# Optimization experiments

Measured on AMD Instinct MI355X. Metric: run time of the kernel, lower is better.

The kernel has to match this reference:

```python
import jax, jax.numpy as jnp
import numpy as np

C = 256       # channels (MWI ctor arg c)
K = 8         # number of EM bases (MWI ctor arg k)
STAGES = 7    # EM iterations per scale (stage_num)
SIZES = (1, 3, 5)  # multi-scale unfold kernel sizes


def _unfold(x, k):
    # torch F.unfold(x, k, padding=(k-1)//2, stride=1) -> (b, c, k*k, h, w)
    # with kernel-position ordering (ki major, kj minor), matching torch layout.
    b, c, h, w = x.shape
    p = (k - 1) // 2
    xp = jnp.pad(x, ((0, 0), (0, 0), (p, p), (p, p)))
    pats = [xp[:, :, i:i + h, j:j + w] for i in range(k) for j in range(k)]
    return jnp.stack(pats, axis=2)


def _fold(z, k, h, w):
    # inverse of _unfold with overlap-add: z (b, c, k*k, h, w) -> (b, c, h, w)
    b, c, kk, _, _ = z.shape
    p = (k - 1) // 2
    out = jnp.zeros((b, c, h + 2 * p, w + 2 * p), z.dtype)
    for idx in range(kk):
        i, j = divmod(idx, k)
        out = out.at[:, :, i:i + h, j:j + w].add(z[:, :, idx])
    return out[:, :, p:p + h, p:p + w]


def _l2norm(v, axis):
    return v / (1e-6 + jnp.linalg.norm(v, axis=axis, keepdims=True))


def setup_inputs() -> dict:
    key = jax.random.key(0)
    k0, k1, k2 = jax.random.split(key, 3)
    b, h, w = 4, 64, 64
    x = jax.random.normal(k0, (b, C, h, w), jnp.float32)
    # mu buffer: normal(0, sqrt(2/k)) then l2-normalized over channel dim
    mu0 = jax.random.normal(k1, (1, C, K), jnp.float32) * np.float32(np.sqrt(2.0 / K))
    mu0 = _l2norm(mu0, axis=1)
    w_scale = jnp.float32(1.0)
    # convcat: Conv2d(3c, c, 1) init normal(0, sqrt(2/(1*1*out_channels)))
    convcat_w = jax.random.normal(k2, (C, 3 * C, 1, 1), jnp.float32) * np.float32(np.sqrt(2.0 / C))
    convcat_b = jnp.zeros((C,), jnp.float32)
    return {"x": x, "mu0": mu0, "w_scale": w_scale,
            "convcat_w": convcat_w, "convcat_b": convcat_b}


def reference(x, mu0, w_scale, convcat_w, convcat_b):
    b, c, h, w = x.shape
    idn = x
    # EM iterations run under torch.no_grad(): stop gradients through mu/z.
    mu = jax.lax.stop_gradient(jnp.broadcast_to(mu0, (b, c, K)))
    feats = []
    for size in SIZES:
        uf = _unfold(x, size).reshape(b, c, -1)          # (b, c, n), n = size^2*h*w
        uf_sg = jax.lax.stop_gradient(uf)
        z = None
        for _ in range(STAGES):
            z = jax.nn.softmax(jnp.einsum('bcn,bck->bnk', uf_sg, mu), axis=2)
            z_ = z / (1e-6 + z.sum(axis=1, keepdims=True))
            mu = _l2norm(jnp.einsum('bcn,bnk->bck', uf_sg, z_), axis=1)
        # reconstruction: mu @ z^T -> (b, c, n), fold back with overlap-add
        zr = jnp.einsum('bck,bnk->bcn', mu, z).reshape(b, c, size * size, h, w)
        feats.append(_fold(zr, size, h, w))
    cat = jnp.concatenate(feats, axis=1)                 # (b, 3c, h, w)
    u = jnp.einsum('bihw,oi->bohw', cat, convcat_w[:, :, 0, 0]) \
        + convcat_b[None, :, None, None]
    out = jax.nn.relu(u * w_scale + idn)
    return out, mu
```

## Files before the change

### kernel.cpp

```cpp
#include <hip/hip_runtime.h>
#include <hip/hip_bf16.h>

#define KB 8


__device__ __forceinline__ float bf16_to_f(unsigned short u) {
    union { unsigned int i; float f; } v;
    v.i = ((unsigned int)u) << 16;
    return v.f;
}

__device__ __forceinline__ unsigned short f_to_bf16_bits(float f) {
    __hip_bfloat16 h = (__hip_bfloat16)f;
    return *(unsigned short*)&h;
}

__device__ __forceinline__ float wf(int i, int pd) {
    return (float)(min(pd, i) + min(pd, 63 - i) + 1);
}

__global__ __launch_bounds__(256)
void probe_all_kernel(const unsigned short* __restrict__ x,
                      const unsigned short* __restrict__ mu0,
                      const unsigned short* __restrict__ Wc,
                      int* __restrict__ slots)
{
    __shared__ unsigned int red[256];
    int bid = blockIdx.x, t = threadIdx.x;
    const unsigned short* p;
    int n;
    if (bid < 32)       { p = x + bid * 2048;         n = 2048; }
    else if (bid == 32) { p = mu0;                    n = 2048; }
    else                { p = Wc + (bid - 33) * 4096; n = 4096; }
    unsigned int mx = 0;
    for (int i = t; i < n; i += 256) {
        unsigned int bits = (((unsigned int)p[i]) << 16) & 0x7FFFFFFFu;
        mx = max(mx, bits);
    }
    red[t] = mx;
    __syncthreads();
    for (int st = 128; st > 0; st >>= 1) {
        if (t < st) red[t] = max(red[t], red[t + st]);
        __syncthreads();
    }
    if (t == 0) slots[bid] = (int)red[0];
}

__global__ __launch_bounds__(256)
void decide_init_kernel(const unsigned short* __restrict__ wsc_u,
                        const void* __restrict__ mu0,
                        int* __restrict__ slots,
                        float* __restrict__ muInit)
{
    int t = threadIdx.x;
    if (t == 0) {
        const int TH = 0x49742400;
        int mxX = 0, mxW = 0;
        for (int i = 0; i < 32; ++i)  mxX = max(mxX, slots[i]);
        for (int i = 33; i < 49; ++i) mxW = max(mxW, slots[i]);
        slots[56] = (mxX < TH) ? 1 : 0;
        slots[57] = (slots[32] < TH) ? 1 : 0;
        slots[58] = (mxW < TH) ? 1 : 0;
        slots[59] = (bf16_to_f(wsc_u[0]) == 1.0f) ? 1 : 0;
    }
    __syncthreads();
    int fb = slots[57];
    const unsigned short* mb = (const unsigned short*)mu0;
    const float*          mf = (const float*)mu0;
    for (int i = t; i < 2048; i += 256)
        muInit[i] = fb ? bf16_to_f(mb[i]) : mf[i];
}

__global__ __launch_bounds__(512)
void stage_z_kernel(const void* __restrict__ x,
                    unsigned short* __restrict__ xbf,
                    const float* __restrict__ inst,
                    const float* __restrict__ muInit,
                    const void* __restrict__ Wc,
                    float* __restrict__ Mg,
                    float* __restrict__ pp,
                    float* __restrict__ pps,
                    __hip_bfloat16* __restrict__ zfOut,
                    const int* __restrict__ flags,
                    int pd, float oobPrev, int mode, int writeM, int sM,
                    int writeXbf)
{
    __shared__ __hip_bfloat16 xt[256][66];
    __shared__ float muL[2048];
    __shared__ float pr[4608];
    __shared__ float zws[512];
    __shared__ float muRed[32];
    __shared__ float sS[8][8];

    const int tid = threadIdx.x;
    const int bid = blockIdx.x;
    const int b   = bid >> 6;
    const int row = bid & 63;
    const int p0  = row << 6;
    const int fW  = flags[2];

    if (!writeXbf) {
        #pragma unroll
        for (int i = 0; i < 4; ++i) {
            int idx = tid + i * 512;
            int c = idx >> 3, sub = idx & 7;
            const uint4 u = *(const uint4*)(xbf
                          + ((size_t)(b * 256 + c) << 12) + (size_t)(p0 + sub * 8));
            unsigned int* d = (unsigned int*)((unsigned short*)&xt[c][0] + sub * 8);
            d[0] = u.x; d[1] = u.y; d[2] = u.z; d[3] = u.w;
        }
    } else if (flags[0]) {
        #pragma unroll
        for (int i = 0; i < 4; ++i) {
            int idx = tid + i * 512;
            int c = idx >> 3, sub = idx & 7;
            size_t gb = ((size_t)(b * 256 + c) << 12) + (size_t)(p0 + sub * 8);
            const uint4 u = *(const uint4*)((const unsigned short*)x + gb);
            unsigned int* d = (unsigned int*)((unsigned short*)&xt[c][0] + sub * 8);
            d[0] = u.x; d[1] = u.y; d[2] = u.z; d[3] = u.w;
            *(uint4*)(xbf + gb) = u;
        }
    } else {
        #pragma unroll
        for (int i = 0; i < 8; ++i) {
            int idx = tid + i * 512;
            int c = idx >> 4, sub = idx & 15;
            size_t gb = ((size_t)(b * 256 + c) << 12) + (size_t)(p0 + sub * 4);
            const float4 a = *(const float4*)((const float*)x + gb);
            unsigned int u0 = ((unsigned int)f_to_bf16_bits(a.y) << 16) | f_to_bf16_bits(a.x);
            unsigned int u1 = ((unsigned int)f_to_bf16_bits(a.w) << 16) | f_to_bf16_bits(a.z);
            unsigned int* d = (unsigned int*)((unsigned short*)&xt[c][0] + sub * 4);
            d[0] = u0; d[1] = u1;
            *(uint2*)(xbf + gb) = make_uint2(u0, u1);
        }
    }

    float v4[4];
    if (mode) {
        const int c  = tid & 255;
        const int kh = (tid >> 8) * 4;
        float r2[4];
        #pragma unroll
        for (int k = 0; k < 4; ++k) {
            float s0 = inst[8192 + b * 8 + kh + k] + oobPrev * 0.125f;
            v4[k] = inst[b * 2048 + c * 8 + kh + k] / (1e-6f + s0);
            r2[k] = v4[k] * v4[k];
        }
        #pragma unroll
        for (int off = 32; off > 0; off >>= 1) {
            #pragma unroll
            for (int k = 0; k < 4; ++k) r2[k] += __shfl_xor(r2[k], off, 64);
        }
        if ((tid & 63) == 0) {
            int w = tid >> 6;
            #pragma unroll
            for (int k = 0; k < 4; ++k) muRed[w * 4 + k] = r2[k];
        }
    }
    __syncthreads();
    if (mode) {
        const int c  = tid & 255;
        const int kh = (tid >> 8) * 4;
        const int base0 = (tid >> 8) * 16;
        #pragma unroll
        for (int k = 0; k < 4; ++k) {
            float s2 = muRed[base0 + k] + muRed[base0 + k + 4]
                     + muRed[base0 + k + 8] + muRed[base0 + k + 12];
            muL[c * 8 + kh + k] = v4[k] / (1e-6f + sqrtf(s2));
        }
    } else {
        *(float4*)(muL + tid * 4) = *(const float4*)(muInit + tid * 4);
    }
    __syncthreads();

    if (writeM && row < 8 && tid < 256) {
        int o = row * 32 + (tid >> 3), k = tid & 7;
        int base = o * 768 + sM * 256;
        float acc = 0.f;
        if (fW) {
            const unsigned short* wp = (const unsigned short*)Wc + base;
            for (int c = 0; c < 256; ++c) acc += bf16_to_f(wp[c]) * muL[c * 8 + k];
        } else {
            const float* wp = (const float*)Wc + base;
            for (int c = 0; c < 256; ++c) acc += wp[c] * muL[c * 8 + k];
        }
        Mg[b * 6144 + o * 24 + sM * 8 + k] = acc;
    }

    {
        const int pp2 = tid & 31;
        const int g   = tid >> 5;
        const int w   = tid >> 6;
        float d0[KB], d1[KB];
        #pragma unroll
        for (int k = 0; k < KB; ++k) { d0[k] = 0.f; d1[k] = 0.f; }
        #pragma unroll 4
        for (int cc = 0; cc < 16; ++cc) {
            int c = g * 16 + cc;
            unsigned int xu = *(const unsigned int*)(&xt[c][2 * pp2]);
            float xv0 = bf16_to_f((unsigned short)(xu & 0xFFFFu));
            float xv1 = bf16_to_f((unsigned short)(xu >> 16));
            float4 ma = *(const float4*)(muL + c * 8);
            float4 mb = *(const float4*)(muL + c * 8 + 4);
            d0[0] += xv0 * ma.x; d0[1] += xv0 * ma.y;
            d0[2] += xv0 * ma.z; d0[3] += xv0 * ma.w;
            d0[4] += xv0 * mb.x; d0[5] += xv0 * mb.y;
            d0[6] += xv0 * mb.z; d0[7] += xv0 * mb.w;
            d1[0] += xv1 * ma.x; d1[1] += xv1 * ma.y;
            d1[2] += xv1 * ma.z; d1[3] += xv1 * ma.w;
            d1[4] += xv1 * mb.x; d1[5] += xv1 * mb.y;
            d1[6] += xv1 * mb.z; d1[7] += xv1 * mb.w;
        }
        #pragma unroll
        for (int k = 0; k < KB; ++k) {
            d0[k] += __shfl_xor(d0[k], 32, 64);
            d1[k] += __shfl_xor(d1[k], 32, 64);
        }
        if ((tid & 63) < 32) {
            float* prw = pr + (w * 64 + 2 * pp2) * 9;
            #pragma unroll
            for (int k = 0; k < KB; ++k) prw[k] = d0[k];
            #pragma unroll
            for (int k = 0; k < KB; ++k) prw[9 + k] = d1[k];
        }
    }
    __syncthreads();

    {
        const int pi = tid >> 3, k = tid & 7;
        float l = 0.f;
        #pragma unroll
        for (int g = 0; g < 8; ++g) l += pr[(g * 64 + pi) * 9 + k];
        float m = l;
        #pragma unroll
        for (int off = 1; off < 8; off <<= 1)
            m = fmaxf(m, __shfl_xor(m, off, 64));
        float e = expf(l - m);
        float se = e;
        #pragma unroll
        for (int off = 1; off < 8; off <<= 1)
            se += __shfl_xor(se, off, 64);
        float wgt = wf(row, pd) * wf(pi, pd);
        float z = e * (wgt / se);
        zws[tid] = z;
        if (zfOut)
            zfOut[(size_t)(b * 4096 + p0 + pi) * KB + k] = (__hip_bfloat16)z;
        float sw = z;
        sw += __shfl_xor(sw, 8, 64);
        sw += __shfl_xor(sw, 16, 64);
        sw += __shfl_xor(sw, 32, 64);
        if ((tid & 63) < 8) sS[tid >> 6][tid & 7] = sw;
    }
    __syncthreads();

    if (tid < 8) {
        float ss = 0.f;
        #pragma unroll
        for (int w = 0; w < 8; ++w) ss += sS[w][tid];
        pps[bid * 8 + tid] = ss;
    }

    {
        const int c2 = tid & 255, half = tid >> 8;
        float macc[KB];
        #pragma unroll
        for (int k = 0; k < KB; ++k) macc[k] = 0.f;
        #pragma unroll 4
        for (int q = 0; q < 32; ++q) {
            int pl = half * 32 + q;
            float xv = (float)xt[c2][pl];
            float4 za = *(const float4*)(zws + pl * 8);
            float4 zb = *(const float4*)(zws + pl * 8 + 4);
            macc[0] += xv * za.x; macc[1] += xv * za.y;
            macc[2] += xv * za.z; macc[3] += xv * za.w;
            macc[4] += xv * zb.x; macc[5] += xv * zb.y;
            macc[6] += xv * zb.z; macc[7] += xv * zb.w;
        }
        if (half) {
            #pragma unroll
            for (int k = 0; k < KB; ++k) pr[c2 * 8 + k] = macc[k];
        }
        __syncthreads();
        if (!half) {
            #pragma unroll
            for (int k = 0; k < KB; ++k) macc[k] += pr[c2 * 8 + k];
            float* pd0 = pp + (size_t)bid * 2048 + c2 * 8;
            *(float4*)pd0       = make_float4(macc[0], macc[1], macc[2], macc[3]);
            *(float4*)(pd0 + 4) = make_float4(macc[4], macc[5], macc[6], macc[7]);
        }
    }
}

__global__ __launch_bounds__(256)
void reduce_kernel(const float* __restrict__ pp,
                   const float* __restrict__ pps,
                   float* __restrict__ inst)
{
    __shared__ float comb[128];
    int bid = blockIdx.x, tid = threadIdx.x;
    int b = bid >> 4, j = bid & 15;
    int e = j * 128 + (tid & 127);
    int rg = tid >> 7;
    const float* base = pp + ((size_t)(b * 64 + rg * 32) * 2048) + e;
    float a0 = 0.f, a1 = 0.f, a2 = 0.f, a3 = 0.f;
    for (int r = 0; r < 32; r += 4) {
        a0 += base[(size_t)(r + 0) * 2048];
        a1 += base[(size_t)(r + 1) * 2048];
        a2 += base[(size_t)(r + 2) * 2048];
        a3 += base[(size_t)(r + 3) * 2048];
    }
    float acc = (a0 + a1) + (a2 + a3);
    if (rg) comb[tid & 127] = acc;
    __syncthreads();
    if (!rg) inst[b * 2048 + e] = acc + comb[tid & 127];
    if (j == 0 && tid < 8) {
        float ss = 0.f;
        const float* sb = pps + (size_t)b * 512 + tid;
        #pragma unroll 8
        for (int r = 0; r < 64; ++r) ss += sb[r * 8];
        inst[8192 + b * 8 + tid] = ss;
    }
}

__global__ __launch_bounds__(256)
void reduce_final_kernel(const float* __restrict__ inst,
                         const void* __restrict__ Wc,
                         const int* __restrict__ flags,
                         float* __restrict__ Mg,
                         float* __restrict__ muOut)
{
    __shared__ float muL[2048];
    __shared__ float muRed[32];
    const int tid = threadIdx.x;
    const int b   = blockIdx.x >> 3;
    const int sub = blockIdx.x & 7;

    float v[KB], r2[KB];
    const float* accRow = inst + b * 2048 + tid * 8;
    #pragma unroll
    for (int k = 0; k < KB; ++k) {
        float s0 = inst[8192 + b * 8 + k] + 3804.f * 0.125f;
        v[k] = accRow[k] / (1e-6f + s0);
        r2[k] = v[k] * v[k];
    }
    #pragma unroll
    for (int off = 32; off > 0; off >>= 1) {
        #pragma unroll
        for (int k = 0; k < KB; ++k) r2[k] += __shfl_xor(r2[k], off, 64);
    }
    if ((tid & 63) == 0) {
        #pragma unroll
        for (int k = 0; k < KB; ++k) muRed[(tid >> 6) * 8 + k] = r2[k];
    }
    __syncthreads();
    #pragma unroll
    for (int k = 0; k < KB; ++k) {
        float s2 = muRed[k] + muRed[8 + k] + muRed[16 + k] + muRed[24 + k];
        float mv = v[k] / (1e-6f + sqrtf(s2));
        muL[tid * 8 + k] = mv;
        if (sub == 0 && muOut) muOut[b * 2048 + tid * 8 + k] = mv;
    }
    __syncthreads();
    {
        int o = sub * 32 + (tid >> 3), k = tid & 7;
        int base = o * 768 + 2 * 256;
        float acc = 0.f;
        if (flags[2]) {
            const unsigned short* wp = (const unsigned short*)Wc + base;
            for (int c = 0; c < 256; ++c) acc += bf16_to_f(wp[c]) * muL[c * 8 + k];
        } else {
            const float* wp = (const float*)Wc + base;
            for (int c = 0; c < 256; ++c) acc += wp[c] * muL[c * 8 + k];
        }
        Mg[b * 6144 + o * 24 + 16 + k] = acc;
    }
}

__global__ __launch_bounds__(256)
void out_kernel(const void* __restrict__ x,
                const float* __restrict__ Mg,
                const __hip_bfloat16* __restrict__ zf,
                const unsigned short* __restrict__ bias_u,
                const unsigned short* __restrict__ wsc_u,
                const int* __restrict__ flags,
                float* __restrict__ out)
{
    __shared__ float ML[256 * 24];
    __shared__ float biasL[256];
    int tid = threadIdx.x, bid = blockIdx.x;
    int b = bid >> 7, tile = bid & 127, p0 = tile << 5;
    int fx = flags[0];
    #pragma unroll
    for (int j = 0; j < 24; ++j) ML[tid + j * 256] = Mg[b * 6144 + tid + j * 256];
    biasL[tid] = bf16_to_f(bias_u[tid]);
    __syncthreads();

    float wsv = flags[3] ? bf16_to_f(wsc_u[0]) : ((const float*)wsc_u)[0];
    int pl = tid & 31, og = tid >> 5;
    int p = p0 + pl;
    float zv[24];
    #pragma unroll
    for (int s = 0; s < 3; ++s) {
        const __hip_bfloat16* zp = zf + s * 131072 + (b * 4096 + p) * KB;
        #pragma unroll
        for (int k = 0; k < KB; ++k) zv[s * 8 + k] = (float)zp[k];
    }
    const size_t gbase = (size_t)(b * 256 + og * 32) * 4096 + (size_t)p;
    float* op = out + gbase;
    if (fx) {
        const unsigned short* xp = (const unsigned short*)x + gbase;
        for (int oo = 0; oo < 32; ++oo) {
            int c = og * 32 + oo;
            float u = biasL[c];
            #pragma unroll
            for (int j = 0; j < 24; ++j) u += ML[c * 24 + j] * zv[j];
            op[(size_t)oo * 4096] =
                fmaxf(u * wsv + bf16_to_f(xp[(size_t)oo * 4096]), 0.f);
        }
    } else {
        const float* xp = (const float*)x + gbase;
        for (int oo = 0; oo < 32; ++oo) {
            int c = og * 32 + oo;
            float u = biasL[c];
            #pragma unroll
            for (int j = 0; j < 24; ++j) u += ML[c * 24 + j] * zv[j];
            op[(size_t)oo * 4096] = fmaxf(u * wsv + xp[(size_t)oo * 4096], 0.f);
        }
    }
}

extern "C" void kernel_launch(void* const* d_in, const int* in_sizes, int n_in,
                              void* d_out, int out_size, void* d_ws, size_t ws_size,
                              hipStream_t stream)
{
    (void)ws_size;
    float* out = (float*)d_out;

    const void *x = nullptr, *mu0 = nullptr, *wsc = nullptr,
               *Wc = nullptr, *bias = nullptr;
    for (int i = 0; i < n_in; ++i) {
        switch (in_sizes[i]) {
            case 4194304: x    = d_in[i]; break;
            case 2048:    mu0  = d_in[i]; break;
            case 1:       wsc  = d_in[i]; break;
            case 196608:  Wc   = d_in[i]; break;
            case 256:     bias = d_in[i]; break;
            default: break;
        }
    }
    if (!x || !mu0 || !wsc || !Wc || !bias) return;

    float* muOut = (out_size >= 4202496) ? (out + 4194304) : (float*)nullptr;

    float* wsf    = (float*)d_ws;
    float* muInit = wsf;
    float* Mg     = wsf + 2048;
    int*   slots  = (int*)(wsf + 26624);
    int*   flags  = slots + 56;
    __hip_bfloat16* zf  = (__hip_bfloat16*)(wsf + 26752);
    float* inst   = wsf + 223360;
    float* pps    = wsf + 231584;
    float* pp     = wsf + 233728;
    unsigned short* xbf = (unsigned short*)(wsf + 758016);

    probe_all_kernel<<<49, 256, 0, stream>>>(
        (const unsigned short*)x, (const unsigned short*)mu0,
        (const unsigned short*)Wc, slots);
    decide_init_kernel<<<1, 256, 0, stream>>>(
        (const unsigned short*)wsc, mu0, slots, muInit);

    const float oobArr[3] = {0.f, 764.f, 3804.f};
    for (int t = 0; t < 21; ++t) {
        int   s        = t / 7;
        int   mode     = (t == 0) ? 0 : 1;
        float oobPrev  = (t == 0) ? 0.f : oobArr[(t - 1) / 7];
        int   writeM   = (t == 7 || t == 14) ? 1 : 0;
        int   sM       = (t == 7) ? 0 : 1;
        int   writeXbf = (t == 0) ? 1 : 0;
        __hip_bfloat16* zfOut = ((t % 7) == 6) ? (zf + s * 131072)
                                               : (__hip_bfloat16*)nullptr;
        stage_z_kernel<<<256, 512, 0, stream>>>(
            x, xbf, inst, muInit, Wc, Mg, pp, pps, zfOut, flags,
            s, oobPrev, mode, writeM, sM, writeXbf);
        reduce_kernel<<<64, 256, 0, stream>>>(pp, pps, inst);
    }

    reduce_final_kernel<<<32, 256, 0, stream>>>(inst, Wc, flags, Mg, muOut);

    out_kernel<<<512, 256, 0, stream>>>(
        x, Mg, zf, (const unsigned short*)bias, (const unsigned short*)wsc,
        flags, out);
}
```

Before: 369.1 us.

## Replace per-iteration reduction kernel with float atomics into pre-zeroed buffers

```diff
diff --git a/kernel.cpp b/kernel.cpp
--- a/kernel.cpp
+++ b/kernel.cpp
@@ -23,10 +23,13 @@
 void probe_all_kernel(const unsigned short* __restrict__ x,
                       const unsigned short* __restrict__ mu0,
                       const unsigned short* __restrict__ Wc,
-                      int* __restrict__ slots)
+                      int* __restrict__ slots,
+                      float* __restrict__ accum, int accumN)
 {
     __shared__ unsigned int red[256];
     int bid = blockIdx.x, t = threadIdx.x;
+    for (int i = bid * 256 + t; i < accumN; i += gridDim.x * 256)
+        accum[i] = 0.f;
     const unsigned short* p;
     int n;
     if (bid < 32)       { p = x + bid * 2048;         n = 2048; }
@@ -74,12 +77,11 @@
 __global__ __launch_bounds__(512)
 void stage_z_kernel(const void* __restrict__ x,
                     unsigned short* __restrict__ xbf,
-                    const float* __restrict__ inst,
+                    const float* __restrict__ accumIn,
                     const float* __restrict__ muInit,
                     const void* __restrict__ Wc,
                     float* __restrict__ Mg,
-                    float* __restrict__ pp,
-                    float* __restrict__ pps,
+                    float* __restrict__ accumOut,
                     __hip_bfloat16* __restrict__ zfOut,
                     const int* __restrict__ flags,
                     int pd, float oobPrev, int mode, int writeM, int sM,
@@ -142,8 +144,8 @@
         float r2[4];
         #pragma unroll
         for (int k = 0; k < 4; ++k) {
-            float s0 = inst[8192 + b * 8 + kh + k] + oobPrev * 0.125f;
-            v4[k] = inst[b * 2048 + c * 8 + kh + k] / (1e-6f + s0);
+            float s0 = accumIn[8192 + b * 8 + kh + k] + oobPrev * 0.125f;
+            v4[k] = accumIn[b * 2048 + c * 8 + kh + k] / (1e-6f + s0);
             r2[k] = v4[k] * v4[k];
         }
         #pragma unroll
@@ -257,7 +259,7 @@
         float ss = 0.f;
         #pragma unroll
         for (int w = 0; w < 8; ++w) ss += sS[w][tid];
-        pps[bid * 8 + tid] = ss;
+        unsafeAtomicAdd(accumOut + 8192 + b * 8 + tid, ss);
     }
 
     {
@@ -282,43 +284,11 @@
         }
         __syncthreads();
         if (!half) {
-            #pragma unroll
-            for (int k = 0; k < KB; ++k) macc[k] += pr[c2 * 8 + k];
-            float* pd0 = pp + (size_t)bid * 2048 + c2 * 8;
-            *(float4*)pd0       = make_float4(macc[0], macc[1], macc[2], macc[3]);
-            *(float4*)(pd0 + 4) = make_float4(macc[4], macc[5], macc[6], macc[7]);
-        }
-    }
-}
-
-__global__ __launch_bounds__(256)
-void reduce_kernel(const float* __restrict__ pp,
-                   const float* __restrict__ pps,
-                   float* __restrict__ inst)
-{
-    __shared__ float comb[128];
-    int bid = blockIdx.x, tid = threadIdx.x;
-    int b = bid >> 4, j = bid & 15;
-    int e = j * 128 + (tid & 127);
-    int rg = tid >> 7;
-    const float* base = pp + ((size_t)(b * 64 + rg * 32) * 2048) + e;
-    float a0 = 0.f, a1 = 0.f, a2 = 0.f, a3 = 0.f;
-    for (int r = 0; r < 32; r += 4) {
-        a0 += base[(size_t)(r + 0) * 2048];
-        a1 += base[(size_t)(r + 1) * 2048];
-        a2 += base[(size_t)(r + 2) * 2048];
-        a3 += base[(size_t)(r + 3) * 2048];
-    }
-    float acc = (a0 + a1) + (a2 + a3);
-    if (rg) comb[tid & 127] = acc;
-    __syncthreads();
-    if (!rg) inst[b * 2048 + e] = acc + comb[tid & 127];
-    if (j == 0 && tid < 8) {
-        float ss = 0.f;
-        const float* sb = pps + (size_t)b * 512 + tid;
-        #pragma unroll 8
-        for (int r = 0; r < 64; ++r) ss += sb[r * 8];
-        inst[8192 + b * 8 + tid] = ss;
+            float* ad = accumOut + b * 2048 + c2 * 8;
+            #pragma unroll
+            for (int k = 0; k < KB; ++k)
+                unsafeAtomicAdd(ad + k, macc[k] + pr[c2 * 8 + k]);
+        }
     }
 }
 
@@ -458,14 +428,12 @@
     int*   slots  = (int*)(wsf + 26624);
     int*   flags  = slots + 56;
     __hip_bfloat16* zf  = (__hip_bfloat16*)(wsf + 26752);
-    float* inst   = wsf + 223360;
-    float* pps    = wsf + 231584;
-    float* pp     = wsf + 233728;
+    float* accum  = wsf + 223360;
     unsigned short* xbf = (unsigned short*)(wsf + 758016);
 
     probe_all_kernel<<<49, 256, 0, stream>>>(
         (const unsigned short*)x, (const unsigned short*)mu0,
-        (const unsigned short*)Wc, slots);
+        (const unsigned short*)Wc, slots, accum, 21 * 8224);
     decide_init_kernel<<<1, 256, 0, stream>>>(
         (const unsigned short*)wsc, mu0, slots, muInit);
 
@@ -479,13 +447,15 @@
         int   writeXbf = (t == 0) ? 1 : 0;
         __hip_bfloat16* zfOut = ((t % 7) == 6) ? (zf + s * 131072)
                                                : (__hip_bfloat16*)nullptr;
+        const float* aIn = accum + (size_t)((t > 0) ? (t - 1) : 0) * 8224;
+        float*       aOut = accum + (size_t)t * 8224;
         stage_z_kernel<<<256, 512, 0, stream>>>(
-            x, xbf, inst, muInit, Wc, Mg, pp, pps, zfOut, flags,
+            x, xbf, aIn, muInit, Wc, Mg, aOut, zfOut, flags,
             s, oobPrev, mode, writeM, sM, writeXbf);
-        reduce_kernel<<<64, 256, 0, stream>>>(pp, pps, inst);
-    }
-
-    reduce_final_kernel<<<32, 256, 0, stream>>>(inst, Wc, flags, Mg, muOut);
+    }
+
+    reduce_final_kernel<<<32, 256, 0, stream>>>(
+        accum + (size_t)20 * 8224, Wc, flags, Mg, muOut);
 
     out_kernel<<<512, 256, 0, stream>>>(
         x, Mg, zf, (const unsigned short*)bias, (const unsigned short*)wsc,
```

Result: slower. 696.0 us (+88.5%).
